# Kernel tuning notes

Hardware: AMD Instinct MI355X
Metric: run time of the kernel (lower is better)

## Reference

```python
import jax, jax.numpy as jnp
import numpy as np

N_NODES = 50000
N_EDGES = 800000
IN_DIM = 256
EDGE_DIM = 64
EMBED = 128
HEADS = 8
HEAD_DIM = EMBED // HEADS


def mish(x):
    return x * jnp.tanh(jax.nn.softplus(x))


def setup_inputs() -> dict:
    key = jax.random.key(0)
    ks = jax.random.split(key, 9)
    return {
        "node_features": jax.random.normal(ks[0], (N_NODES, IN_DIM), jnp.float32),
        "edge_features": jax.random.normal(ks[1], (N_EDGES, EDGE_DIM), jnp.float32),
        "W_kernel": jax.random.normal(ks[2], (IN_DIM, EMBED), jnp.float32) * (1.0 / np.sqrt(IN_DIM)),
        "W_bias": jax.random.normal(ks[3], (EMBED,), jnp.float32) * 0.01,
        "We_kernel": jax.random.normal(ks[4], (EDGE_DIM, EMBED), jnp.float32) * (1.0 / np.sqrt(EDGE_DIM)),
        "We_bias": jax.random.normal(ks[5], (EMBED,), jnp.float32) * 0.01,
        "a": jax.random.normal(ks[6], (HEADS, HEAD_DIM), jnp.float32) * (1.0 / np.sqrt(HEAD_DIM)),
        "senders": jax.random.randint(ks[7], (N_EDGES,), 0, N_NODES, jnp.int32),
        "receivers": jax.random.randint(ks[8], (N_EDGES,), 0, N_NODES, jnp.int32),
    }


def reference(node_features, edge_features, W_kernel, W_bias, We_kernel, We_bias, a, senders, receivers):
    num_nodes = node_features.shape[-2]
    # shared projection (share_weights=True): h_send == h_recv
    h = node_features @ W_kernel + W_bias                      # [N, D]
    e_send = h[senders]                                        # [E, D] gather
    e_recv = h[receivers]                                      # [E, D] gather
    e_attn = e_send + e_recv + (edge_features @ We_kernel + We_bias)
    e_attn = mish(e_attn).reshape(-1, HEADS, HEAD_DIM)         # [E, H, Dh]
    logits = jnp.einsum('ehd,hd->eh', e_attn, a)               # [E, H]
    # segment softmax over receiver groups
    seg_max = jax.ops.segment_max(logits, receivers, num_segments=num_nodes)  # [N, H]
    ex = jnp.exp(logits - seg_max[receivers])
    denom = jax.ops.segment_sum(ex, receivers, num_segments=num_nodes)
    weights = ex / denom[receivers]                            # [E, H]
    # weighted scatter-sum of sender features
    msg = (weights[..., None] * e_send.reshape(-1, HEADS, HEAD_DIM)).reshape(-1, EMBED)
    nodes = jax.ops.segment_sum(msg, receivers, num_segments=num_nodes)       # [N, D]
    return nodes
```

## Files before the change

### kernel.cpp

```cpp
#include <hip/hip_runtime.h>
#include <math.h>

#define NN 50000
#define NE 800000
#define IND 256
#define ED 64
#define EMB 128
#define NH 8
#define HD 16

typedef short bf16x8 __attribute__((ext_vector_type(8)));
typedef float f32x4 __attribute__((ext_vector_type(4)));

#define NPT  (NN / 16)
#define NPB  ((NPT + 3) / 4)
#define NHIST ((NE + 255) / 256)
#define NB   ((NN + 511) / 512)

__device__ __forceinline__ unsigned short rne16(float f) {
    unsigned u = __float_as_uint(f);
    unsigned r = u + 0x7FFFu + ((u >> 16) & 1u);
    return (unsigned short)(r >> 16);
}

__device__ __forceinline__ float bf2f(short s) {
    return __uint_as_float(((unsigned)(unsigned short)s) << 16);
}

__device__ __forceinline__ float mishf(float v) {
    float t = __expf(fminf(v, 20.f));
    float u = 1.f + t;
    u = u * u;
    return v * (u - 1.f) * __builtin_amdgcn_rcpf(u + 1.f);
}

__global__ __launch_bounds__(256) void k_proj_hist(
    const float* __restrict__ X, const float* __restrict__ W,
    const float* __restrict__ b, short* __restrict__ hbf,
    const int* __restrict__ rcv, int* __restrict__ cnt) {
    if (blockIdx.x >= NPB) {
        int e = (blockIdx.x - NPB) * 256 + threadIdx.x;
        if (e < NE) atomicAdd(&cnt[rcv[e]], 1);
        return;
    }
    __shared__ short BHs[IND * EMB];
    for (int idx = threadIdx.x * 4; idx < IND * EMB; idx += 256 * 4) {
        float4 wv = *(const float4*)&W[idx];
        int k = idx >> 7;
        int col = idx & 127;
        int kk8 = k >> 5, qq = (k & 31) >> 3, j = k & 7;
        float wf[4] = {wv.x, wv.y, wv.z, wv.w};
        #pragma unroll
        for (int i = 0; i < 4; ++i) {
            int cc = (col + i) & 7, lc = (col + i) >> 3;
            int lane = (qq << 4) | lc;
            BHs[(((cc << 3) | kk8) * 64 + lane) * 8 + j] = (short)rne16(wf[i]);
        }
    }
    __syncthreads();

    const int l = threadIdx.x & 63;
    const int lanecol = l & 15;
    const int q = l >> 4;
    const int wid = (blockIdx.x << 2) + (threadIdx.x >> 6);
    const int nW = NPB << 2;

    float4 bv0 = *(const float4*)&b[lanecol * 8];
    float4 bv1 = *(const float4*)&b[lanecol * 8 + 4];
    float wb[8] = {bv0.x, bv0.y, bv0.z, bv0.w, bv1.x, bv1.y, bv1.z, bv1.w};

    for (int tIdx = wid; tIdx < NPT; tIdx += nW) {
        const int n0 = tIdx * 16;
        f32x4 acc[8];
        #pragma unroll
        for (int c = 0; c < 8; ++c) acc[c] = (f32x4){0.f, 0.f, 0.f, 0.f};
        #pragma unroll
        for (int kk8 = 0; kk8 < 8; ++kk8) {
            const float* ar = X + (size_t)(n0 + lanecol) * IND + kk8 * 32 + q * 8;
            float4 a0 = *(const float4*)ar;
            float4 a1 = *(const float4*)(ar + 4);
            float faf[8] = {a0.x, a0.y, a0.z, a0.w, a1.x, a1.y, a1.z, a1.w};
            bf16x8 ahi;
            #pragma unroll
            for (int j = 0; j < 8; ++j) ahi[j] = (short)rne16(faf[j]);
            #pragma unroll
            for (int c = 0; c < 8; ++c) {
                bf16x8 bh = *(bf16x8*)&BHs[(((c << 3) | kk8) * 64 + l) * 8];
                acc[c] = __builtin_amdgcn_mfma_f32_16x16x32_bf16(ahi, bh, acc[c], 0, 0, 0);
            }
        }
        #pragma unroll
        for (int r = 0; r < 4; ++r) {
            const int node = n0 + (q << 2) + r;
            bf16x8 ov;
            #pragma unroll
            for (int c = 0; c < 8; ++c) ov[c] = (short)rne16(acc[c][r] + wb[c]);
            *(bf16x8*)(hbf + (size_t)node * EMB + lanecol * 8) = ov;
        }
    }
}

__global__ __launch_bounds__(512) void k_part(const int* __restrict__ cnt,
                                              int* __restrict__ rowptr,
                                              int* __restrict__ part) {
    __shared__ int sm[512];
    const int t = threadIdx.x;
    const int idx = blockIdx.x * 512 + t;
    int v = (idx < NN) ? cnt[idx] : 0;
    sm[t] = v;
    __syncthreads();
    #pragma unroll
    for (int off = 1; off < 512; off <<= 1) {
        int y = (t >= off) ? sm[t - off] : 0;
        __syncthreads();
        sm[t] += y;
        __syncthreads();
    }
    if (idx < NN) rowptr[idx] = sm[t] - v;
    if (t == 511) part[blockIdx.x] = sm[511];
}

__global__ __launch_bounds__(512) void k_fix2(const int* __restrict__ part,
                                              int* __restrict__ rowptr,
                                              int* __restrict__ cursor) {
    __shared__ int sm[128];
    const int t = threadIdx.x;
    if (t < 128) sm[t] = (t < NB) ? part[t] : 0;
    __syncthreads();
    #pragma unroll
    for (int off = 1; off < 128; off <<= 1) {
        int y = 0;
        if (t < 128 && t >= off) y = sm[t - off];
        __syncthreads();
        if (t < 128) sm[t] += y;
        __syncthreads();
    }
    const int boff = (blockIdx.x > 0) ? sm[blockIdx.x - 1] : 0;
    const int idx = blockIdx.x * 512 + t;
    if (idx < NN) {
        int r = rowptr[idx] + boff;
        rowptr[idx] = r;
        cursor[idx] = r;
    }
    if (blockIdx.x == 0 && t == 0) rowptr[NN] = NE;
}

__global__ __launch_bounds__(256) void k_edge_attn(
    const float* __restrict__ EF, const float* __restrict__ We,
    const float* __restrict__ Web, const float* __restrict__ Av,
    const short* __restrict__ hbf, const int* __restrict__ snd,
    const int* __restrict__ rcv, int* __restrict__ cursor,
    int* __restrict__ csr_snd, float* __restrict__ ex_csr) {
    __shared__ short BHs[ED * EMB];
    __shared__ float2 WA[144];
    for (int idx = threadIdx.x * 4; idx < ED * EMB; idx += 256 * 4) {
        float4 wv = *(const float4*)&We[idx];
        int k = idx >> 7;
        int col = idx & 127;
        int kk = k >> 5, qq = (k & 31) >> 3, j = k & 7;
        float wf[4] = {wv.x, wv.y, wv.z, wv.w};
        #pragma unroll
        for (int i = 0; i < 4; ++i) {
            int cc = (col + i) & 7, lc = (col + i) >> 3;
            int lane = (qq << 4) | lc;
            BHs[(((cc << 1) | kk) * 64 + lane) * 8 + j] = (short)rne16(wf[i]);
        }
    }
    if (threadIdx.x < 128) {
        int c = threadIdx.x & 7, lc = threadIdx.x >> 3;
        WA[lc * 9 + c] = make_float2(Web[threadIdx.x], Av[threadIdx.x]);
    }
    __syncthreads();

    const int l = threadIdx.x & 63;
    const int lanecol = l & 15;
    const int q = l >> 4;
    const int gbase = l & 48;
    const int wid = (blockIdx.x << 2) + (threadIdx.x >> 6);
    const int nW = gridDim.x << 2;
    const int NT = NE / 16;

    for (int tIdx = wid; tIdx < NT; tIdx += nW) {
        const int e0 = tIdx * 16;
        const int eb = e0 + (q << 2);

        int4 s4 = *(const int4*)&snd[eb];
        int4 r4 = *(const int4*)&rcv[eb];

        bf16x8 hsv0 = *(const bf16x8*)(hbf + (size_t)s4.x * EMB + lanecol * 8);
        bf16x8 hrv0 = *(const bf16x8*)(hbf + (size_t)r4.x * EMB + lanecol * 8);
        bf16x8 hsv1 = *(const bf16x8*)(hbf + (size_t)s4.y * EMB + lanecol * 8);
        bf16x8 hrv1 = *(const bf16x8*)(hbf + (size_t)r4.y * EMB + lanecol * 8);
        bf16x8 hsv2 = *(const bf16x8*)(hbf + (size_t)s4.z * EMB + lanecol * 8);
        bf16x8 hrv2 = *(const bf16x8*)(hbf + (size_t)r4.z * EMB + lanecol * 8);
        bf16x8 hsv3 = *(const bf16x8*)(hbf + (size_t)s4.w * EMB + lanecol * 8);
        bf16x8 hrv3 = *(const bf16x8*)(hbf + (size_t)r4.w * EMB + lanecol * 8);

        int ssel = (lanecol == 0) ? s4.x : (lanecol == 1) ? s4.y
                 : (lanecol == 2) ? s4.z : s4.w;
        int rsel = (lanecol == 0) ? r4.x : (lanecol == 1) ? r4.y
                 : (lanecol == 2) ? r4.z : r4.w;
        int pos4 = 0;
        if (lanecol < 4) {
            pos4 = atomicAdd(&cursor[rsel], 1);
            csr_snd[pos4] = ssel;
        }

        const float* ar = EF + (size_t)(e0 + lanecol) * ED + q * 8;
        bf16x8 ahi0, ahi1;
        {
            float4 a0 = *(const float4*)ar;
            float4 a1 = *(const float4*)(ar + 4);
            float4 a2 = *(const float4*)(ar + 32);
            float4 a3 = *(const float4*)(ar + 36);
            ahi0[0] = (short)rne16(a0.x); ahi0[1] = (short)rne16(a0.y);
            ahi0[2] = (short)rne16(a0.z); ahi0[3] = (short)rne16(a0.w);
            ahi0[4] = (short)rne16(a1.x); ahi0[5] = (short)rne16(a1.y);
            ahi0[6] = (short)rne16(a1.z); ahi0[7] = (short)rne16(a1.w);
            ahi1[0] = (short)rne16(a2.x); ahi1[1] = (short)rne16(a2.y);
            ahi1[2] = (short)rne16(a2.z); ahi1[3] = (short)rne16(a2.w);
            ahi1[4] = (short)rne16(a3.x); ahi1[5] = (short)rne16(a3.y);
            ahi1[6] = (short)rne16(a3.z); ahi1[7] = (short)rne16(a3.w);
        }

        float pp[4] = {0.f, 0.f, 0.f, 0.f};
        #pragma unroll
        for (int c = 0; c < 8; ++c) {
            bf16x8 b0 = *(bf16x8*)&BHs[(((c << 1) | 0) * 64 + l) * 8];
            bf16x8 b1 = *(bf16x8*)&BHs[(((c << 1) | 1) * 64 + l) * 8];
            f32x4 a4 = (f32x4){0.f, 0.f, 0.f, 0.f};
            a4 = __builtin_amdgcn_mfma_f32_16x16x32_bf16(ahi0, b0, a4, 0, 0, 0);
            a4 = __builtin_amdgcn_mfma_f32_16x16x32_bf16(ahi1, b1, a4, 0, 0, 0);
            float2 wa = WA[lanecol * 9 + c];
            pp[0] = fmaf(mishf(a4[0] + wa.x + bf2f(hsv0[c]) + bf2f(hrv0[c])), wa.y, pp[0]);
            pp[1] = fmaf(mishf(a4[1] + wa.x + bf2f(hsv1[c]) + bf2f(hrv1[c])), wa.y, pp[1]);
            pp[2] = fmaf(mishf(a4[2] + wa.x + bf2f(hsv2[c]) + bf2f(hrv2[c])), wa.y, pp[2]);
            pp[3] = fmaf(mishf(a4[3] + wa.x + bf2f(hsv3[c]) + bf2f(hrv3[c])), wa.y, pp[3]);
        }

        #pragma unroll
        for (int r = 0; r < 4; ++r) {
            float pr = pp[r];
            pr += __shfl_xor(pr, 1, 16);
            const int pos = __shfl(pos4, gbase + r, 64);
            if ((lanecol & 1) == 0)
                ex_csr[(size_t)pos * NH + (lanecol >> 1)] = __expf(pr);
        }
    }
}

__global__ __launch_bounds__(256) void k_agg(
    const short* __restrict__ hbf, const int* __restrict__ csr_snd,
    const float* __restrict__ ex_csr, const int* __restrict__ rowptr,
    float* __restrict__ out) {
    const int l = threadIdx.x & 63;
    const int node = blockIdx.x * 4 + (threadIdx.x >> 6);
    if (node >= NN) return;
    const int beg = rowptr[node], end = rowptr[node + 1];
    const int h = l >> 3;
    float a0 = 0.f, a1 = 0.f, den = 0.f;
    int j = beg;
    for (; j + 4 <= end; j += 4) {
        int s[4];
        float ex[4];
        unsigned hv[4];
        #pragma unroll
        for (int i = 0; i < 4; ++i) s[i] = csr_snd[j + i];
        #pragma unroll
        for (int i = 0; i < 4; ++i) ex[i] = ex_csr[(size_t)(j + i) * NH + h];
        #pragma unroll
        for (int i = 0; i < 4; ++i)
            hv[i] = *(const unsigned*)(hbf + (size_t)s[i] * EMB + 2 * l);
        #pragma unroll
        for (int i = 0; i < 4; ++i) {
            a0 = fmaf(ex[i], bf2f((short)(hv[i] & 0xFFFF)), a0);
            a1 = fmaf(ex[i], bf2f((short)(hv[i] >> 16)), a1);
            den += ex[i];
        }
    }
    for (; j < end; ++j) {
        float ex = ex_csr[(size_t)j * NH + h];
        unsigned hv = *(const unsigned*)(hbf + (size_t)csr_snd[j] * EMB + 2 * l);
        a0 = fmaf(ex, bf2f((short)(hv & 0xFFFF)), a0);
        a1 = fmaf(ex, bf2f((short)(hv >> 16)), a1);
        den += ex;
    }
    float rd = (end > beg) ? __builtin_amdgcn_rcpf(den) : 0.f;
    float2 o;
    o.x = a0 * rd;
    o.y = a1 * rd;
    *(float2*)&out[(size_t)node * EMB + 2 * l] = o;
}

extern "C" void kernel_launch(void* const* d_in, const int* in_sizes, int n_in,
                              void* d_out, int out_size, void* d_ws, size_t ws_size,
                              hipStream_t stream) {
    const float* X   = (const float*)d_in[0];
    const float* EF  = (const float*)d_in[1];
    const float* W   = (const float*)d_in[2];
    const float* Wb  = (const float*)d_in[3];
    const float* We  = (const float*)d_in[4];
    const float* Web = (const float*)d_in[5];
    const float* Av  = (const float*)d_in[6];
    const int* snd   = (const int*)d_in[7];
    const int* rcv   = (const int*)d_in[8];
    float* out = (float*)d_out;

    char* ws = (char*)d_ws;
    size_t off = 0;
    float* ex_csr = (float*)(ws + off); off += (size_t)NE * NH * 4;
    int* csr_snd  = (int*)(ws + off);   off += (size_t)NE * 4;
    int* rowptr   = (int*)(ws + off);   off += (size_t)(NN + 1) * 4;
    int* cursor   = (int*)(ws + off);   off += (size_t)NN * 4;
    int* part     = (int*)(ws + off);   off += 512;
    short* hbf    = (short*)(ws + off); off += (size_t)NN * EMB * 2;
    int* cnt      = cursor;

    hipMemsetAsync(cnt, 0, (size_t)NN * sizeof(int), stream);
    k_proj_hist<<<NPB + NHIST, 256, 0, stream>>>(X, W, Wb, hbf, rcv, cnt);
    k_part<<<NB, 512, 0, stream>>>(cnt, rowptr, part);
    k_fix2<<<NB, 512, 0, stream>>>(part, rowptr, cursor);
    k_edge_attn<<<2048, 256, 0, stream>>>(EF, We, Web, Av, hbf, snd, rcv,
                                          cursor, csr_snd, ex_csr);
    k_agg<<<(NN + 3) / 4, 256, 0, stream>>>(hbf, csr_snd, ex_csr, rowptr, out);
}
```

Before: 250.7 us.

## Bucket edges by receiver before attention; store exp weights in bf16

Adds a separate bucketing kernel that scatters (edge, sender, receiver) records into CSR order. The attention kernel then processes edges in receiver-sorted order, reading edge features through an indirection and writing exp weights contiguously as bf16. This gives better locality for receiver gathers and smaller writes. The aggregation loop is unrolled to 8 and reads senders from the 16-byte records. The trade-offs are an extra kernel launch, 16-byte record traffic, a scattered read of edge features, and lower precision in the weights.

```diff
diff --git a/kernel.cpp b/kernel.cpp
--- a/kernel.cpp
+++ b/kernel.cpp
@@ -23,8 +23,8 @@
     return (unsigned short)(r >> 16);
 }
 
-__device__ __forceinline__ float bf2f(short s) {
-    return __uint_as_float(((unsigned)(unsigned short)s) << 16);
+__device__ __forceinline__ float bf2f(unsigned short s) {
+    return __uint_as_float(((unsigned)s) << 16);
 }
 
 __device__ __forceinline__ float mishf(float v) {
@@ -145,12 +145,22 @@
     if (blockIdx.x == 0 && t == 0) rowptr[NN] = NE;
 }
 
+__global__ __launch_bounds__(256) void k_bucket(
+    const int* __restrict__ snd, const int* __restrict__ rcv,
+    int* __restrict__ cursor, int4* __restrict__ rec) {
+    int e = blockIdx.x * 256 + threadIdx.x;
+    if (e < NE) {
+        int r = rcv[e];
+        int pos = atomicAdd(&cursor[r], 1);
+        rec[pos] = make_int4(e, snd[e], r, 0);
+    }
+}
+
 __global__ __launch_bounds__(256) void k_edge_attn(
     const float* __restrict__ EF, const float* __restrict__ We,
     const float* __restrict__ Web, const float* __restrict__ Av,
-    const short* __restrict__ hbf, const int* __restrict__ snd,
-    const int* __restrict__ rcv, int* __restrict__ cursor,
-    int* __restrict__ csr_snd, float* __restrict__ ex_csr) {
+    const short* __restrict__ hbf, const int4* __restrict__ rec,
+    unsigned short* __restrict__ exbf) {
     __shared__ short BHs[ED * EMB];
     __shared__ float2 WA[144];
     for (int idx = threadIdx.x * 4; idx < ED * EMB; idx += 256 * 4) {
@@ -175,38 +185,32 @@
     const int l = threadIdx.x & 63;
     const int lanecol = l & 15;
     const int q = l >> 4;
-    const int gbase = l & 48;
     const int wid = (blockIdx.x << 2) + (threadIdx.x >> 6);
     const int nW = gridDim.x << 2;
     const int NT = NE / 16;
 
     for (int tIdx = wid; tIdx < NT; tIdx += nW) {
-        const int e0 = tIdx * 16;
-        const int eb = e0 + (q << 2);
-
-        int4 s4 = *(const int4*)&snd[eb];
-        int4 r4 = *(const int4*)&rcv[eb];
-
-        bf16x8 hsv0 = *(const bf16x8*)(hbf + (size_t)s4.x * EMB + lanecol * 8);
-        bf16x8 hrv0 = *(const bf16x8*)(hbf + (size_t)r4.x * EMB + lanecol * 8);
-        bf16x8 hsv1 = *(const bf16x8*)(hbf + (size_t)s4.y * EMB + lanecol * 8);
-        bf16x8 hrv1 = *(const bf16x8*)(hbf + (size_t)r4.y * EMB + lanecol * 8);
-        bf16x8 hsv2 = *(const bf16x8*)(hbf + (size_t)s4.z * EMB + lanecol * 8);
-        bf16x8 hrv2 = *(const bf16x8*)(hbf + (size_t)r4.z * EMB + lanecol * 8);
-        bf16x8 hsv3 = *(const bf16x8*)(hbf + (size_t)s4.w * EMB + lanecol * 8);
-        bf16x8 hrv3 = *(const bf16x8*)(hbf + (size_t)r4.w * EMB + lanecol * 8);
-
-        int ssel = (lanecol == 0) ? s4.x : (lanecol == 1) ? s4.y
-                 : (lanecol == 2) ? s4.z : s4.w;
-        int rsel = (lanecol == 0) ? r4.x : (lanecol == 1) ? r4.y
-                 : (lanecol == 2) ? r4.z : r4.w;
-        int pos4 = 0;
-        if (lanecol < 4) {
-            pos4 = atomicAdd(&cursor[rsel], 1);
-            csr_snd[pos4] = ssel;
-        }
-
-        const float* ar = EF + (size_t)(e0 + lanecol) * ED + q * 8;
+        int4 rc = rec[(size_t)tIdx * 16 + lanecol];
+
+        int se0 = __shfl(rc.y, (q << 2) + 0, 16);
+        int re0 = __shfl(rc.z, (q << 2) + 0, 16);
+        int se1 = __shfl(rc.y, (q << 2) + 1, 16);
+        int re1 = __shfl(rc.z, (q << 2) + 1, 16);
+        int se2 = __shfl(rc.y, (q << 2) + 2, 16);
+        int re2 = __shfl(rc.z, (q << 2) + 2, 16);
+        int se3 = __shfl(rc.y, (q << 2) + 3, 16);
+        int re3 = __shfl(rc.z, (q << 2) + 3, 16);
+
+        bf16x8 hsv0 = *(const bf16x8*)(hbf + (size_t)se0 * EMB + lanecol * 8);
+        bf16x8 hrv0 = *(const bf16x8*)(hbf + (size_t)re0 * EMB + lanecol * 8);
+        bf16x8 hsv1 = *(const bf16x8*)(hbf + (size_t)se1 * EMB + lanecol * 8);
+        bf16x8 hrv1 = *(const bf16x8*)(hbf + (size_t)re1 * EMB + lanecol * 8);
+        bf16x8 hsv2 = *(const bf16x8*)(hbf + (size_t)se2 * EMB + lanecol * 8);
+        bf16x8 hrv2 = *(const bf16x8*)(hbf + (size_t)re2 * EMB + lanecol * 8);
+        bf16x8 hsv3 = *(const bf16x8*)(hbf + (size_t)se3 * EMB + lanecol * 8);
+        bf16x8 hrv3 = *(const bf16x8*)(hbf + (size_t)re3 * EMB + lanecol * 8);
+
+        const float* ar = EF + (size_t)rc.x * ED + q * 8;
         bf16x8 ahi0, ahi1;
         {
             float4 a0 = *(const float4*)ar;
@@ -232,26 +236,26 @@
             a4 = __builtin_amdgcn_mfma_f32_16x16x32_bf16(ahi0, b0, a4, 0, 0, 0);
             a4 = __builtin_amdgcn_mfma_f32_16x16x32_bf16(ahi1, b1, a4, 0, 0, 0);
             float2 wa = WA[lanecol * 9 + c];
-            pp[0] = fmaf(mishf(a4[0] + wa.x + bf2f(hsv0[c]) + bf2f(hrv0[c])), wa.y, pp[0]);
-            pp[1] = fmaf(mishf(a4[1] + wa.x + bf2f(hsv1[c]) + bf2f(hrv1[c])), wa.y, pp[1]);
-            pp[2] = fmaf(mishf(a4[2] + wa.x + bf2f(hsv2[c]) + bf2f(hrv2[c])), wa.y, pp[2]);
-            pp[3] = fmaf(mishf(a4[3] + wa.x + bf2f(hsv3[c]) + bf2f(hrv3[c])), wa.y, pp[3]);
+            pp[0] = fmaf(mishf(a4[0] + wa.x + bf2f((unsigned short)hsv0[c]) + bf2f((unsigned short)hrv0[c])), wa.y, pp[0]);
+            pp[1] = fmaf(mishf(a4[1] + wa.x + bf2f((unsigned short)hsv1[c]) + bf2f((unsigned short)hrv1[c])), wa.y, pp[1]);
+            pp[2] = fmaf(mishf(a4[2] + wa.x + bf2f((unsigned short)hsv2[c]) + bf2f((unsigned short)hrv2[c])), wa.y, pp[2]);
+            pp[3] = fmaf(mishf(a4[3] + wa.x + bf2f((unsigned short)hsv3[c]) + bf2f((unsigned short)hrv3[c])), wa.y, pp[3]);
         }
 
         #pragma unroll
         for (int r = 0; r < 4; ++r) {
             float pr = pp[r];
             pr += __shfl_xor(pr, 1, 16);
-            const int pos = __shfl(pos4, gbase + r, 64);
+            const size_t pos = (size_t)tIdx * 16 + (q << 2) + r;
             if ((lanecol & 1) == 0)
-                ex_csr[(size_t)pos * NH + (lanecol >> 1)] = __expf(pr);
+                exbf[pos * NH + (lanecol >> 1)] = rne16(__expf(pr));
         }
     }
 }
 
 __global__ __launch_bounds__(256) void k_agg(
-    const short* __restrict__ hbf, const int* __restrict__ csr_snd,
-    const float* __restrict__ ex_csr, const int* __restrict__ rowptr,
+    const short* __restrict__ hbf, const int4* __restrict__ rec,
+    const unsigned short* __restrict__ exbf, const int* __restrict__ rowptr,
     float* __restrict__ out) {
     const int l = threadIdx.x & 63;
     const int node = blockIdx.x * 4 + (threadIdx.x >> 6);
@@ -260,29 +264,29 @@
     const int h = l >> 3;
     float a0 = 0.f, a1 = 0.f, den = 0.f;
     int j = beg;
-    for (; j + 4 <= end; j += 4) {
-        int s[4];
-        float ex[4];
-        unsigned hv[4];
-        #pragma unroll
-        for (int i = 0; i < 4; ++i) s[i] = csr_snd[j + i];
-        #pragma unroll
-        for (int i = 0; i < 4; ++i) ex[i] = ex_csr[(size_t)(j + i) * NH + h];
-        #pragma unroll
-        for (int i = 0; i < 4; ++i)
+    for (; j + 8 <= end; j += 8) {
+        int s[8];
+        float ex[8];
+        unsigned hv[8];
+        #pragma unroll
+        for (int i = 0; i < 8; ++i) s[i] = rec[j + i].y;
+        #pragma unroll
+        for (int i = 0; i < 8; ++i) ex[i] = bf2f(exbf[(size_t)(j + i) * NH + h]);
+        #pragma unroll
+        for (int i = 0; i < 8; ++i)
             hv[i] = *(const unsigned*)(hbf + (size_t)s[i] * EMB + 2 * l);
         #pragma unroll
-        for (int i = 0; i < 4; ++i) {
-            a0 = fmaf(ex[i], bf2f((short)(hv[i] & 0xFFFF)), a0);
-            a1 = fmaf(ex[i], bf2f((short)(hv[i] >> 16)), a1);
+        for (int i = 0; i < 8; ++i) {
+            a0 = fmaf(ex[i], bf2f((unsigned short)(hv[i] & 0xFFFF)), a0);
+            a1 = fmaf(ex[i], bf2f((unsigned short)(hv[i] >> 16)), a1);
             den += ex[i];
         }
     }
     for (; j < end; ++j) {
-        float ex = ex_csr[(size_t)j * NH + h];
-        unsigned hv = *(const unsigned*)(hbf + (size_t)csr_snd[j] * EMB + 2 * l);
-        a0 = fmaf(ex, bf2f((short)(hv & 0xFFFF)), a0);
-        a1 = fmaf(ex, bf2f((short)(hv >> 16)), a1);
+        float ex = bf2f(exbf[(size_t)j * NH + h]);
+        unsigned hv = *(const unsigned*)(hbf + (size_t)rec[j].y * EMB + 2 * l);
+        a0 = fmaf(ex, bf2f((unsigned short)(hv & 0xFFFF)), a0);
+        a1 = fmaf(ex, bf2f((unsigned short)(hv >> 16)), a1);
         den += ex;
     }
     float rd = (end > beg) ? __builtin_amdgcn_rcpf(den) : 0.f;
@@ -308,8 +312,8 @@
 
     char* ws = (char*)d_ws;
     size_t off = 0;
-    float* ex_csr = (float*)(ws + off); off += (size_t)NE * NH * 4;
-    int* csr_snd  = (int*)(ws + off);   off += (size_t)NE * 4;
+    unsigned short* exbf = (unsigned short*)(ws + off); off += (size_t)NE * NH * 2;
+    int4* rec     = (int4*)(ws + off);  off += (size_t)NE * 16;
     int* rowptr   = (int*)(ws + off);   off += (size_t)(NN + 1) * 4;
     int* cursor   = (int*)(ws + off);   off += (size_t)NN * 4;
     int* part     = (int*)(ws + off);   off += 512;
@@ -320,7 +324,7 @@
     k_proj_hist<<<NPB + NHIST, 256, 0, stream>>>(X, W, Wb, hbf, rcv, cnt);
     k_part<<<NB, 512, 0, stream>>>(cnt, rowptr, part);
     k_fix2<<<NB, 512, 0, stream>>>(part, rowptr, cursor);
-    k_edge_attn<<<2048, 256, 0, stream>>>(EF, We, Web, Av, hbf, snd, rcv,
-                                          cursor, csr_snd, ex_csr);
-    k_agg<<<(NN + 3) / 4, 256, 0, stream>>>(hbf, csr_snd, ex_csr, rowptr, out);
-}
+    k_bucket<<<NHIST, 256, 0, stream>>>(snd, rcv, cursor, rec);
+    k_edge_attn<<<2048, 256, 0, stream>>>(EF, We, Web, Av, hbf, rec, exbf);
+    k_agg<<<(NN + 3) / 4, 256, 0, stream>>>(hbf, rec, exbf, rowptr, out);
+}
```

New measurement: 281.5 us. 12.3% more time.
